# Kernel optimization log

Measured on AMD Instinct MI355X. Metric: run time of the kernel, lower is better.

Reference implementation:

```python
import jax, jax.numpy as jnp
import numpy as np

NUM_HEADS = 12
HEAD_DIM = 64
LMBDA = 0.01
BLIND_SPOT = True


def setup_inputs() -> dict:
    key = jax.random.key(0)
    ks = jax.random.split(key, 4)
    B, S, D = 8, 1024, 768
    scale = 1.0 / np.sqrt(D)
    return {
        "hidden_states": jax.random.normal(ks[0], (B, S, D), jnp.float32),
        "attention_mask": jnp.zeros((B, 1, 1, S), jnp.float32),
        "Wq": jax.random.normal(ks[1], (D, D), jnp.float32) * scale,
        "bq": jnp.zeros((D,), jnp.float32),
        "Wk": jax.random.normal(ks[2], (D, D), jnp.float32) * scale,
        "bk": jnp.zeros((D,), jnp.float32),
        "Wv": jax.random.normal(ks[3], (D, D), jnp.float32) * scale,
        "bv": jnp.zeros((D,), jnp.float32),
    }


def _split_heads(x):
    B, S, D = x.shape
    return x.reshape(B, S, NUM_HEADS, HEAD_DIM).transpose(0, 2, 1, 3)  # [B,H,S,dh]


def reference(hidden_states, attention_mask, Wq, bq, Wk, bk, Wv, bv):
    B, S, D = hidden_states.shape
    q = _split_heads(hidden_states @ Wq + bq)
    k = _split_heads(hidden_states @ Wk + bk)
    v = _split_heads(hidden_states @ Wv + bv)

    scores = jnp.einsum("bhqd,bhkd->bhqk", q, k)  # [B,H,S,S]
    if BLIND_SPOT:
        # zero out the diagonal BEFORE scaling (matches original order)
        eye = jnp.eye(S, dtype=scores.dtype)
        scores = scores * (1.0 - eye)
    scores = scores / np.sqrt(HEAD_Dim() if False else HEAD_DIM).astype(np.float32)
    scores = scores + attention_mask  # additive mask, broadcast [B,1,1,S]

    # auxiliary diagonal-weighted regularization loss
    if LMBDA != 0.0:
        diag_vals = jnp.diagonal(scores, axis1=-2, axis2=-1)  # [B,H,S]
        loss = LMBDA * jnp.sum(diag_vals)
    else:
        loss = jnp.float32(0.0)

    probs = jax.nn.softmax(scores, axis=-1)  # dropout = identity (eval)
    context = jnp.einsum("bhqk,bhkd->bhqd", probs, v)  # [B,H,S,dh]
    context = context.transpose(0, 2, 1, 3).reshape(B, S, D)
    return context, loss
```

## Files before the change

### kernel.cpp

```cpp
#include <hip/hip_runtime.h>
#include <hip/hip_bf16.h>
#include <stdint.h>

#define Bb 8
#define Ss 1024
#define Dd 768
#define Hh 12
#define DH 64

typedef __attribute__((ext_vector_type(8))) short bf16x8;
typedef __attribute__((ext_vector_type(4))) float f32x4;

static __device__ __forceinline__ unsigned short f2b(float x) {
    union { float f; unsigned u; } v; v.f = x;
    unsigned r = v.u + 0x7FFFu + ((v.u >> 16) & 1u);
    return (unsigned short)(r >> 16);
}

static __device__ __forceinline__ void gll16(const void* g, void* l) {
    __builtin_amdgcn_global_load_lds((const __attribute__((address_space(1))) void*)g,
                                     (__attribute__((address_space(3))) void*)l,
                                     16, 0, 0);
}

__global__ __launch_bounds__(256) void k_cvt(const float* __restrict__ in,
                                             unsigned short* __restrict__ out) {
    int i = (blockIdx.x * 256 + threadIdx.x) * 4;
    const float4 v = *reinterpret_cast<const float4*>(in + i);
    ushort4 o;
    o.x = f2b(v.x); o.y = f2b(v.y); o.z = f2b(v.z); o.w = f2b(v.w);
    *reinterpret_cast<ushort4*>(out + i) = o;
}

__global__ __launch_bounds__(256) void k_twt(const float* __restrict__ Wq,
                                             const float* __restrict__ Wk,
                                             const float* __restrict__ Wv,
                                             unsigned short* __restrict__ Wt) {
    __shared__ float tile[32][33];
    const int w = blockIdx.z;
    const float* W = (w == 0) ? Wq : (w == 1) ? Wk : Wv;
    const int k0 = blockIdx.x * 32, n0 = blockIdx.y * 32;
    const int c = threadIdx.x & 31, r0 = threadIdx.x >> 5;
    #pragma unroll
    for (int i = 0; i < 4; ++i)
        tile[r0 + i * 8][c] = W[(size_t)(k0 + r0 + i * 8) * Dd + n0 + c];
    __syncthreads();
    unsigned short* o = Wt + (size_t)w * Dd * Dd;
    #pragma unroll
    for (int i = 0; i < 4; ++i)
        o[(size_t)(n0 + r0 + i * 8) * Dd + k0 + c] = f2b(tile[c][r0 + i * 8]);
}

__global__ __launch_bounds__(256) void k_qkv(
    const unsigned short* __restrict__ hb,
    const unsigned short* __restrict__ Wt,
    const float* __restrict__ bq, const float* __restrict__ bk, const float* __restrict__ bv,
    unsigned short* __restrict__ Qo, unsigned short* __restrict__ Ko,
    unsigned short* __restrict__ Vo) {
    __shared__ __align__(16) unsigned short Al[128 * 32];
    __shared__ __align__(16) unsigned short Bl[128 * 32];
    const int m0 = blockIdx.x * 128;
    const int n0 = blockIdx.y * 128;
    const int w  = blockIdx.z;
    const int tid = threadIdx.x, lane = tid & 63, wv = tid >> 6;
    const int l15 = lane & 15, l4 = lane >> 4;
    const int wm = (wv >> 1) * 64, wn = (wv & 1) * 64;
    const unsigned short* Wb = Wt + (size_t)w * Dd * Dd;

    f32x4 acc[4][4];
    #pragma unroll
    for (int i = 0; i < 4; ++i)
        #pragma unroll
        for (int j = 0; j < 4; ++j)
            acc[i][j] = f32x4{0.f, 0.f, 0.f, 0.f};

    const int ldr = lane >> 2;
    const int ldc = (lane & 3) * 8;

    for (int kt = 0; kt < Dd / 32; ++kt) {
        const int k0 = kt * 32;
        #pragma unroll
        for (int i = 0; i < 2; ++i) {
            const int c = wv * 2 + i;
            gll16(hb + (size_t)(m0 + c * 16 + ldr) * Dd + k0 + ldc, Al + c * 512);
            gll16(Wb + (size_t)(n0 + c * 16 + ldr) * Dd + k0 + ldc, Bl + c * 512);
        }
        __syncthreads();
        bf16x8 af[4], bfr[4];
        #pragma unroll
        for (int i = 0; i < 4; ++i) {
            af[i]  = *reinterpret_cast<const bf16x8*>(Al + (wm + i * 16 + l15) * 32 + l4 * 8);
            bfr[i] = *reinterpret_cast<const bf16x8*>(Bl + (wn + i * 16 + l15) * 32 + l4 * 8);
        }
        #pragma unroll
        for (int i = 0; i < 4; ++i)
            #pragma unroll
            for (int j = 0; j < 4; ++j)
                acc[i][j] = __builtin_amdgcn_mfma_f32_16x16x32_bf16(af[i], bfr[j], acc[i][j], 0, 0, 0);
        __syncthreads();
    }

    const float* bias = (w == 0) ? bq : (w == 1) ? bk : bv;
    if (w < 2) {
        unsigned short* O = (w == 0) ? Qo : Ko;
        #pragma unroll
        for (int j = 0; j < 4; ++j) {
            const int n = n0 + wn + j * 16 + l15;
            const float bs = bias[n];
            const int hh = n >> 6, d = n & 63;
            #pragma unroll
            for (int i = 0; i < 4; ++i) {
                const int mb = m0 + wm + i * 16 + l4 * 4;
                #pragma unroll
                for (int r = 0; r < 4; ++r) {
                    const int m = mb + r;
                    const int b = m >> 10, s = m & 1023;
                    O[(((size_t)b * Hh + hh) * Ss + s) * DH + d] = f2b(acc[i][j][r] + bs);
                }
            }
        }
    } else {
        #pragma unroll
        for (int j = 0; j < 4; ++j) {
            const int n = n0 + wn + j * 16 + l15;
            const float bs = bias[n];
            const int hh = n >> 6, d = n & 63;
            #pragma unroll
            for (int i = 0; i < 4; ++i) {
                const int m = m0 + wm + i * 16 + l4 * 4;
                const int b = m >> 10, s = m & 1023;
                ushort4 o;
                o.x = f2b(acc[i][j][0] + bs);
                o.y = f2b(acc[i][j][1] + bs);
                o.z = f2b(acc[i][j][2] + bs);
                o.w = f2b(acc[i][j][3] + bs);
                *reinterpret_cast<ushort4*>(Vo + (((size_t)b * Hh + hh) * DH + d) * Ss + s) = o;
            }
        }
    }
}

__global__ __launch_bounds__(256) void k_attn(
    const unsigned short* __restrict__ Q,
    const unsigned short* __restrict__ K,
    const unsigned short* __restrict__ VT,
    const float* __restrict__ mask,
    float* __restrict__ out) {
    __shared__ __align__(16) unsigned short Kl[64 * 64];
    __shared__ __align__(16) unsigned short Vl[64 * 64];
    __shared__ __align__(16) unsigned short Pl[4][16][72];
    const int bh = blockIdx.x;
    const int qt = blockIdx.y;
    const int b = bh / Hh, h = bh % Hh;
    const int tid = threadIdx.x, lane = tid & 63, wv = tid >> 6;
    const int l15 = lane & 15, l4 = lane >> 4;
    const int q0 = qt * 64 + wv * 16;

    const unsigned short* Qb = Q + (size_t)bh * Ss * DH;
    const unsigned short* Kb = K + (size_t)bh * Ss * DH;
    const unsigned short* Vb = VT + (size_t)bh * DH * Ss;
    const float* mb = mask + (size_t)b * Ss;

    const bf16x8 qf0 = *reinterpret_cast<const bf16x8*>(Qb + (q0 + l15) * DH + l4 * 8);
    const bf16x8 qf1 = *reinterpret_cast<const bf16x8*>(Qb + (q0 + l15) * DH + 32 + l4 * 8);

    float m_run[4], l_run[4];
    f32x4 oacc[4];
    #pragma unroll
    for (int r = 0; r < 4; ++r) { m_run[r] = -3.0e38f; l_run[r] = 0.f; }
    #pragma unroll
    for (int dt = 0; dt < 4; ++dt) oacc[dt] = f32x4{0.f, 0.f, 0.f, 0.f};

    const int ldr = lane >> 3, ldc = (lane & 7) * 8;

    for (int kt = 0; kt < Ss / 64; ++kt) {
        #pragma unroll
        for (int i = 0; i < 2; ++i) {
            const int c = wv * 2 + i;
            gll16(Kb + (size_t)(kt * 64 + c * 8 + ldr) * DH + ldc, Kl + c * 512);
            gll16(Vb + (size_t)(c * 8 + ldr) * Ss + kt * 64 + ldc, Vl + c * 512);
        }
        __syncthreads();

        f32x4 sc[4];
        #pragma unroll
        for (int ct = 0; ct < 4; ++ct) {
            const bf16x8 kf0 = *reinterpret_cast<const bf16x8*>(Kl + (ct * 16 + l15) * 64 + l4 * 8);
            const bf16x8 kf1 = *reinterpret_cast<const bf16x8*>(Kl + (ct * 16 + l15) * 64 + 32 + l4 * 8);
            f32x4 a = f32x4{0.f, 0.f, 0.f, 0.f};
            a = __builtin_amdgcn_mfma_f32_16x16x32_bf16(qf0, kf0, a, 0, 0, 0);
            a = __builtin_amdgcn_mfma_f32_16x16x32_bf16(qf1, kf1, a, 0, 0, 0);
            sc[ct] = a;
        }

        float mk[4];
        #pragma unroll
        for (int ct = 0; ct < 4; ++ct) mk[ct] = mb[kt * 64 + ct * 16 + l15];

        float p[4][4];
        #pragma unroll
        for (int r = 0; r < 4; ++r) {
            const int qrow = q0 + l4 * 4 + r;
            float mx = -3.0e38f;
            #pragma unroll
            for (int ct = 0; ct < 4; ++ct) {
                const int kcol = kt * 64 + ct * 16 + l15;
                float s = sc[ct][r] * 0.125f + mk[ct];
                if (kcol == qrow) s = mk[ct];
                p[r][ct] = s;
                mx = fmaxf(mx, s);
            }
            #pragma unroll
            for (int d = 1; d < 16; d <<= 1) mx = fmaxf(mx, __shfl_xor(mx, d));
            const float mnew = fmaxf(m_run[r], mx);
            const float alpha = __expf(m_run[r] - mnew);
            float rsum = 0.f;
            #pragma unroll
            for (int ct = 0; ct < 4; ++ct) {
                const float e = __expf(p[r][ct] - mnew);
                p[r][ct] = e;
                rsum += e;
            }
            #pragma unroll
            for (int d = 1; d < 16; d <<= 1) rsum += __shfl_xor(rsum, d);
            m_run[r] = mnew;
            l_run[r] = l_run[r] * alpha + rsum;
            #pragma unroll
            for (int dt = 0; dt < 4; ++dt) oacc[dt][r] *= alpha;
        }

        #pragma unroll
        for (int r = 0; r < 4; ++r)
            #pragma unroll
            for (int ct = 0; ct < 4; ++ct)
                Pl[wv][l4 * 4 + r][ct * 16 + l15] = f2b(p[r][ct]);

        #pragma unroll
        for (int half = 0; half < 2; ++half) {
            const bf16x8 pf = *reinterpret_cast<const bf16x8*>(&Pl[wv][l15][half * 32 + l4 * 8]);
            #pragma unroll
            for (int dt = 0; dt < 4; ++dt) {
                const bf16x8 vf = *reinterpret_cast<const bf16x8*>(Vl + (dt * 16 + l15) * 64 + half * 32 + l4 * 8);
                oacc[dt] = __builtin_amdgcn_mfma_f32_16x16x32_bf16(pf, vf, oacc[dt], 0, 0, 0);
            }
        }
        __syncthreads();
    }

    #pragma unroll
    for (int r = 0; r < 4; ++r) {
        const float inv = 1.f / l_run[r];
        const int s = q0 + l4 * 4 + r;
        float* op = out + ((size_t)b * Ss + s) * Dd + h * DH;
        #pragma unroll
        for (int dt = 0; dt < 4; ++dt)
            op[dt * 16 + l15] = oacc[dt][r] * inv;
    }
}

__global__ __launch_bounds__(256) void k_loss(const float* __restrict__ mask,
                                              float* __restrict__ out) {
    __shared__ float red[4];
    float s = 0.f;
    for (int i = threadIdx.x; i < Bb * Ss; i += 256) s += mask[i];
    #pragma unroll
    for (int d = 1; d < 64; d <<= 1) s += __shfl_xor(s, d);
    const int lane = threadIdx.x & 63, wv = threadIdx.x >> 6;
    if (lane == 0) red[wv] = s;
    __syncthreads();
    if (threadIdx.x == 0)
        out[0] = 0.01f * 12.f * (red[0] + red[1] + red[2] + red[3]);
}

extern "C" void kernel_launch(void* const* d_in, const int* in_sizes, int n_in,
                              void* d_out, int out_size, void* d_ws, size_t ws_size,
                              hipStream_t stream) {
    const float* hs   = (const float*)d_in[0];
    const float* mask = (const float*)d_in[1];
    const float* Wq   = (const float*)d_in[2];
    const float* bq   = (const float*)d_in[3];
    const float* Wk   = (const float*)d_in[4];
    const float* bk   = (const float*)d_in[5];
    const float* Wv   = (const float*)d_in[6];
    const float* bv   = (const float*)d_in[7];
    float* out = (float*)d_out;

    uint8_t* ws = (uint8_t*)d_ws;
    unsigned short* hb = (unsigned short*)(ws);
    unsigned short* Wt = (unsigned short*)(ws + 12582912);
    unsigned short* Qw = (unsigned short*)(ws + 16121856);
    unsigned short* Kw = (unsigned short*)(ws + 28704768);
    unsigned short* Vw = (unsigned short*)(ws + 41287680);

    hipLaunchKernelGGL(k_cvt,  dim3(6144),       dim3(256), 0, stream, hs, hb);
    hipLaunchKernelGGL(k_twt,  dim3(24, 24, 3),  dim3(256), 0, stream, Wq, Wk, Wv, Wt);
    hipLaunchKernelGGL(k_qkv,  dim3(64, 6, 3),   dim3(256), 0, stream, hb, Wt, bq, bk, bv, Qw, Kw, Vw);
    hipLaunchKernelGGL(k_attn, dim3(96, 16),     dim3(256), 0, stream, Qw, Kw, Vw, mask, out);
    hipLaunchKernelGGL(k_loss, dim3(1),          dim3(256), 0, stream, mask, out + 6291456);
}
```

Baseline: 255.4 us.

## Restructure attention softmax with transposed scores, lazy rescale, and direct K/V loads

The attention kernel swaps the MFMA operand order so each lane holds a row of scores, which cuts the per-row 16-lane shuffle reductions down to two shuffles. It moves the softmax to exp2 with the mask pre-scaled in LDS, and rescales the running max only when a wave's new max exceeds the old one by more than a threshold. K and V tiles are now read straight from global memory instead of being staged through LDS, which removes both per-tile barriers. The grid is reordered so blocks of the same head launch together and share K/V in cache. The risks are redundant global K/V traffic across the four waves, and extra reliance on L2 hit rates in place of shared-memory reuse.

```diff
diff --git a/kernel.cpp b/kernel.cpp
--- a/kernel.cpp
+++ b/kernel.cpp
@@ -146,11 +146,10 @@
     const unsigned short* __restrict__ VT,
     const float* __restrict__ mask,
     float* __restrict__ out) {
-    __shared__ __align__(16) unsigned short Kl[64 * 64];
-    __shared__ __align__(16) unsigned short Vl[64 * 64];
+    __shared__ __align__(16) float Ml[1024];
     __shared__ __align__(16) unsigned short Pl[4][16][72];
-    const int bh = blockIdx.x;
-    const int qt = blockIdx.y;
+    const int qt = blockIdx.x;
+    const int bh = blockIdx.y;
     const int b = bh / Hh, h = bh % Hh;
     const int tid = threadIdx.x, lane = tid & 63, wv = tid >> 6;
     const int l15 = lane & 15, l4 = lane >> 4;
@@ -161,96 +160,110 @@
     const unsigned short* Vb = VT + (size_t)bh * DH * Ss;
     const float* mb = mask + (size_t)b * Ss;
 
+    {
+        const float4 mv = *reinterpret_cast<const float4*>(mb + tid * 4);
+        float4 ms;
+        ms.x = mv.x * 1.44269504f; ms.y = mv.y * 1.44269504f;
+        ms.z = mv.z * 1.44269504f; ms.w = mv.w * 1.44269504f;
+        *reinterpret_cast<float4*>(&Ml[tid * 4]) = ms;
+    }
+    __syncthreads();
+
     const bf16x8 qf0 = *reinterpret_cast<const bf16x8*>(Qb + (q0 + l15) * DH + l4 * 8);
     const bf16x8 qf1 = *reinterpret_cast<const bf16x8*>(Qb + (q0 + l15) * DH + 32 + l4 * 8);
 
-    float m_run[4], l_run[4];
+    float m2 = -3.0e38f, lsum = 0.f;
     f32x4 oacc[4];
     #pragma unroll
-    for (int r = 0; r < 4; ++r) { m_run[r] = -3.0e38f; l_run[r] = 0.f; }
-    #pragma unroll
     for (int dt = 0; dt < 4; ++dt) oacc[dt] = f32x4{0.f, 0.f, 0.f, 0.f};
 
-    const int ldr = lane >> 3, ldc = (lane & 7) * 8;
+    const float C1 = 0.125f * 1.44269504f;
 
     for (int kt = 0; kt < Ss / 64; ++kt) {
-        #pragma unroll
-        for (int i = 0; i < 2; ++i) {
-            const int c = wv * 2 + i;
-            gll16(Kb + (size_t)(kt * 64 + c * 8 + ldr) * DH + ldc, Kl + c * 512);
-            gll16(Vb + (size_t)(c * 8 + ldr) * Ss + kt * 64 + ldc, Vl + c * 512);
-        }
-        __syncthreads();
-
+        const unsigned short* Kt = Kb + (size_t)kt * 64 * DH;
         f32x4 sc[4];
         #pragma unroll
         for (int ct = 0; ct < 4; ++ct) {
-            const bf16x8 kf0 = *reinterpret_cast<const bf16x8*>(Kl + (ct * 16 + l15) * 64 + l4 * 8);
-            const bf16x8 kf1 = *reinterpret_cast<const bf16x8*>(Kl + (ct * 16 + l15) * 64 + 32 + l4 * 8);
+            const bf16x8 kf0 = *reinterpret_cast<const bf16x8*>(Kt + (ct * 16 + l15) * DH + l4 * 8);
+            const bf16x8 kf1 = *reinterpret_cast<const bf16x8*>(Kt + (ct * 16 + l15) * DH + 32 + l4 * 8);
             f32x4 a = f32x4{0.f, 0.f, 0.f, 0.f};
-            a = __builtin_amdgcn_mfma_f32_16x16x32_bf16(qf0, kf0, a, 0, 0, 0);
-            a = __builtin_amdgcn_mfma_f32_16x16x32_bf16(qf1, kf1, a, 0, 0, 0);
+            a = __builtin_amdgcn_mfma_f32_16x16x32_bf16(kf0, qf0, a, 0, 0, 0);
+            a = __builtin_amdgcn_mfma_f32_16x16x32_bf16(kf1, qf1, a, 0, 0, 0);
             sc[ct] = a;
         }
 
-        float mk[4];
-        #pragma unroll
-        for (int ct = 0; ct < 4; ++ct) mk[ct] = mb[kt * 64 + ct * 16 + l15];
-
-        float p[4][4];
-        #pragma unroll
-        for (int r = 0; r < 4; ++r) {
-            const int qrow = q0 + l4 * 4 + r;
-            float mx = -3.0e38f;
-            #pragma unroll
-            for (int ct = 0; ct < 4; ++ct) {
-                const int kcol = kt * 64 + ct * 16 + l15;
-                float s = sc[ct][r] * 0.125f + mk[ct];
-                if (kcol == qrow) s = mk[ct];
-                p[r][ct] = s;
-                mx = fmaxf(mx, s);
+        float4 mk[4];
+        #pragma unroll
+        for (int ct = 0; ct < 4; ++ct)
+            mk[ct] = *reinterpret_cast<const float4*>(&Ml[kt * 64 + ct * 16 + l4 * 4]);
+
+        float p[16];
+        float pmax = -3.0e38f;
+        const bool dk = (kt == qt);
+        #pragma unroll
+        for (int ct = 0; ct < 4; ++ct) {
+            const float* mkp = reinterpret_cast<const float*>(&mk[ct]);
+            #pragma unroll
+            for (int r = 0; r < 4; ++r) {
+                float t = fmaf(sc[ct][r], C1, mkp[r]);
+                if (dk && (ct * 16 + l4 * 4 + r) == (wv * 16 + l15)) t = mkp[r];
+                p[ct * 4 + r] = t;
+                pmax = fmaxf(pmax, t);
             }
-            #pragma unroll
-            for (int d = 1; d < 16; d <<= 1) mx = fmaxf(mx, __shfl_xor(mx, d));
-            const float mnew = fmaxf(m_run[r], mx);
-            const float alpha = __expf(m_run[r] - mnew);
-            float rsum = 0.f;
-            #pragma unroll
-            for (int ct = 0; ct < 4; ++ct) {
-                const float e = __expf(p[r][ct] - mnew);
-                p[r][ct] = e;
-                rsum += e;
-            }
-            #pragma unroll
-            for (int d = 1; d < 16; d <<= 1) rsum += __shfl_xor(rsum, d);
-            m_run[r] = mnew;
-            l_run[r] = l_run[r] * alpha + rsum;
-            #pragma unroll
-            for (int dt = 0; dt < 4; ++dt) oacc[dt][r] *= alpha;
-        }
-
-        #pragma unroll
-        for (int r = 0; r < 4; ++r)
-            #pragma unroll
-            for (int ct = 0; ct < 4; ++ct)
-                Pl[wv][l4 * 4 + r][ct * 16 + l15] = f2b(p[r][ct]);
-
-        #pragma unroll
-        for (int half = 0; half < 2; ++half) {
-            const bf16x8 pf = *reinterpret_cast<const bf16x8*>(&Pl[wv][l15][half * 32 + l4 * 8]);
-            #pragma unroll
-            for (int dt = 0; dt < 4; ++dt) {
-                const bf16x8 vf = *reinterpret_cast<const bf16x8*>(Vl + (dt * 16 + l15) * 64 + half * 32 + l4 * 8);
-                oacc[dt] = __builtin_amdgcn_mfma_f32_16x16x32_bf16(pf, vf, oacc[dt], 0, 0, 0);
-            }
-        }
-        __syncthreads();
+        }
+        pmax = fmaxf(pmax, __shfl_xor(pmax, 16));
+        pmax = fmaxf(pmax, __shfl_xor(pmax, 32));
+
+        if (__any(pmax > m2 + 10.f)) {
+            const float mnew = fmaxf(m2, pmax);
+            const float alpha = __builtin_amdgcn_exp2f(m2 - mnew);
+            m2 = mnew;
+            lsum *= alpha;
+            float ar[4];
+            #pragma unroll
+            for (int r = 0; r < 4; ++r) ar[r] = __shfl(alpha, l4 * 4 + r);
+            #pragma unroll
+            for (int dt = 0; dt < 4; ++dt)
+                #pragma unroll
+                for (int r = 0; r < 4; ++r) oacc[dt][r] *= ar[r];
+        }
+
+        float rs = 0.f;
+        #pragma unroll
+        for (int i = 0; i < 16; ++i) {
+            const float e = __builtin_amdgcn_exp2f(p[i] - m2);
+            p[i] = e;
+            rs += e;
+        }
+        rs += __shfl_xor(rs, 16);
+        rs += __shfl_xor(rs, 32);
+        lsum += rs;
+
+        #pragma unroll
+        for (int ct = 0; ct < 4; ++ct) {
+            unsigned lo, hi;
+            asm("v_cvt_pk_bf16_f32 %0, %1, %2" : "=v"(lo) : "v"(p[ct * 4 + 0]), "v"(p[ct * 4 + 1]));
+            asm("v_cvt_pk_bf16_f32 %0, %1, %2" : "=v"(hi) : "v"(p[ct * 4 + 2]), "v"(p[ct * 4 + 3]));
+            *reinterpret_cast<uint2*>(&Pl[wv][l15][ct * 16 + l4 * 4]) = make_uint2(lo, hi);
+        }
+
+        const bf16x8 pf0 = *reinterpret_cast<const bf16x8*>(&Pl[wv][l15][l4 * 8]);
+        const bf16x8 pf1 = *reinterpret_cast<const bf16x8*>(&Pl[wv][l15][32 + l4 * 8]);
+        const unsigned short* Vt = Vb + kt * 64;
+        #pragma unroll
+        for (int dt = 0; dt < 4; ++dt) {
+            const bf16x8 vf0 = *reinterpret_cast<const bf16x8*>(Vt + (size_t)(dt * 16 + l15) * Ss + l4 * 8);
+            const bf16x8 vf1 = *reinterpret_cast<const bf16x8*>(Vt + (size_t)(dt * 16 + l15) * Ss + 32 + l4 * 8);
+            oacc[dt] = __builtin_amdgcn_mfma_f32_16x16x32_bf16(pf0, vf0, oacc[dt], 0, 0, 0);
+            oacc[dt] = __builtin_amdgcn_mfma_f32_16x16x32_bf16(pf1, vf1, oacc[dt], 0, 0, 0);
+        }
     }
 
     #pragma unroll
     for (int r = 0; r < 4; ++r) {
-        const float inv = 1.f / l_run[r];
-        const int s = q0 + l4 * 4 + r;
+        const float li = __shfl(lsum, l4 * 4 + r);
+        const float inv = 1.f / li;
+        const int s = qt * 64 + wv * 16 + l4 * 4 + r;
         float* op = out + ((size_t)b * Ss + s) * Dd + h * DH;
         #pragma unroll
         for (int dt = 0; dt < 4; ++dt)
@@ -292,9 +305,9 @@
     unsigned short* Kw = (unsigned short*)(ws + 28704768);
     unsigned short* Vw = (unsigned short*)(ws + 41287680);
 
-    hipLaunchKernelGGL(k_cvt,  dim3(6144),       dim3(256), 0, stream, hs, hb);
-    hipLaunchKernelGGL(k_twt,  dim3(24, 24, 3),  dim3(256), 0, stream, Wq, Wk, Wv, Wt);
-    hipLaunchKernelGGL(k_qkv,  dim3(64, 6, 3),   dim3(256), 0, stream, hb, Wt, bq, bk, bv, Qw, Kw, Vw);
-    hipLaunchKernelGGL(k_attn, dim3(96, 16),     dim3(256), 0, stream, Qw, Kw, Vw, mask, out);
-    hipLaunchKernelGGL(k_loss, dim3(1),          dim3(256), 0, stream, mask, out + 6291456);
-}
+    hipLaunchKernelGGL(k_cvt,  dim3(6144),      dim3(256), 0, stream, hs, hb);
+    hipLaunchKernelGGL(k_twt,  dim3(24, 24, 3), dim3(256), 0, stream, Wq, Wk, Wv, Wt);
+    hipLaunchKernelGGL(k_qkv,  dim3(64, 6, 3),  dim3(256), 0, stream, hb, Wt, bq, bk, bv, Qw, Kw, Vw);
+    hipLaunchKernelGGL(k_attn, dim3(16, 96),    dim3(256), 0, stream, Qw, Kw, Vw, mask, out);
+    hipLaunchKernelGGL(k_loss, dim3(1),         dim3(256), 0, stream, mask, out + 6291456);
+}
```

After: 328.5 us. 1.29x slower.
